# Optimization experiments

Hardware: AMD Instinct MI355X
Metric: run time of the kernel (lower is better)

The kernel has to match this reference:

```python
import jax, jax.numpy as jnp
import numpy as np

NB, NX, NU, NY, NQ = 16384, 512, 256, 128, 256


def setup_inputs() -> dict:
    key = jax.random.key(0)
    ks = jax.random.split(key, 13)
    s = 0.02  # small weight scale keeps the tanh recurrence well-behaved
    x = jax.random.normal(ks[0], (NB, NX), jnp.float32)
    u = jax.random.normal(ks[1], (NB, NU), jnp.float32)
    F = jax.random.normal(ks[2], (NX, NX), jnp.float32) * s
    B1 = jax.random.normal(ks[3], (NX, NQ), jnp.float32) * s
    B2 = jax.random.normal(ks[4], (NX, NU), jnp.float32) * s
    C1 = jax.random.normal(ks[5], (NQ, NX), jnp.float32) * s
    C2 = jax.random.normal(ks[6], (NY, NX), jnp.float32) * s
    D11 = jax.random.normal(ks[7], (NQ, NQ), jnp.float32) * s
    D12 = jax.random.normal(ks[8], (NQ, NU), jnp.float32) * s
    D21 = jax.random.normal(ks[9], (NY, NQ), jnp.float32) * s
    # E must be invertible (torch.inverse(self.E)); identity + small perturbation
    E = jnp.eye(NX, dtype=jnp.float32) + 0.05 * jax.random.normal(ks[10], (NX, NX), jnp.float32)
    # Lambda diagonal, positive (only Lambda[k,k] is used in _solve_w)
    lam = jax.random.uniform(ks[11], (NQ,), jnp.float32, minval=0.5, maxval=1.5)
    bv = jnp.zeros((NQ,), jnp.float32)  # bias=False -> bv is zeros
    return dict(x=x, u=u, F=F, B1=B1, B2=B2, C1=C1, C2=C2, D11=D11,
                D12=D12, D21=D21, E=E, lam=lam, bv=bv)


def _solve_w(x, u, C1, D11, D12, lam, bv):
    # Sequential forward-substitution over the nq nonlinear states:
    #   v_k = (x@C1[k] + w@D11[k] + u@D12[k] + bv[k]) / Lambda[k,k];  w_k = tanh(v_k)
    nb = x.shape[0]
    nq = lam.shape[0]
    # x/u contributions do not depend on w: precompute once. [nb, nq]
    xu = x @ C1.T + u @ D12.T + bv[None, :]

    def step(w, inp):
        d11_row, xu_k, lam_k, k = inp
        v_k = (xu_k + w @ d11_row) / lam_k          # [nb]
        w = w.at[:, k].set(jnp.tanh(v_k))
        return w, None

    w0 = jnp.zeros((nb, nq), x.dtype)
    w, _ = jax.lax.scan(step, w0, (D11, xu.T, lam, jnp.arange(nq)))
    return w


def reference(x, u, F, B1, B2, C1, C2, D11, D12, D21, E, lam, bv):
    w = _solve_w(x, u, C1, D11, D12, lam, bv)
    E_inv = jnp.linalg.inv(E)
    dx = x @ (E_inv @ F).T + w @ (E_inv @ B1).T + u @ (E_inv @ B2).T
    # linear_output path (no feedthrough: D22 term omitted as in default D22=0)
    y = x @ C2.T + w @ D21.T
    return dx, y
```

## Files before the change

kernel.cpp:

```cpp
#include <hip/hip_runtime.h>

#define NBq 16384
#define NXq 512
#define NUq 256
#define NYq 128
#define NQq 256
#define KP  1024
#define AUGW 1536

typedef __attribute__((ext_vector_type(8))) short short8;
typedef __attribute__((ext_vector_type(4))) float f32x4;

__device__ __forceinline__ ushort f2bf(float f) {
  uint x = __float_as_uint(f);
  x += 0x7FFFu + ((x >> 16) & 1u);
  return (ushort)(x >> 16);
}

#define GLOAD_LDS16(g, l)                                             \
  __builtin_amdgcn_global_load_lds(                                   \
      (const __attribute__((address_space(1))) void*)(g),             \
      (__attribute__((address_space(3))) void*)(l), 16, 0, 0)

__device__ __forceinline__ float rdlane(float x, int l) {
// ... 24 lines not shown
      int row = i >> 6, c4 = i & 63;
      ushort4 h = { f2bf(v.x), f2bf(v.y), f2bf(v.z), f2bf(v.w) };
      *(ushort4*)(P + (size_t)row * KP + 768 + c4 * 4) = h;
    }
  } else if (b < 15360) {
    int idx = (b - 12288) * 256 + tid;
    int r = idx / AUGW, c = idx % AUGW;
    float v;
    if (c < 512)       v = E[r * 512 + c];
    else if (c < 1024) v = F[r * 512 + (c - 512)];
    else if (c < 1280) v = B1[r * 256 + (c - 1024)];
    else               v = B2[r * 256 + (c - 1280)];
    AUG[idx] = v;
  } else if (b < 16384) {
    int idx = (b - 15360) * 256 + tid;
    int r = idx >> 10, k = idx & 1023;
    float v;
    if (k < 512)      v = C1[r * 512 + k];
    else if (k < 768) v = 0.f;
    else              v = D12[r * 256 + (k - 768)];
    Wxu[idx] = f2bf(v);
  } else if (b < 16640) {
    int idx = (b - 16384) * 256 + tid;
    D11B[idx] = f2bf(D11[idx]);
  } else {
    int idx = (b - 16640) * 256 + tid;
    int j = idx >> 10, k = idx & 1023;
    float v;
    if (k < 512)      v = C2[j * 512 + k];
    else if (k < 768) v = D21[j * 256 + (k - 512)];
    else              v = 0.f;
    Wfull[(size_t)(512 + j) * KP + k] = f2bf(v);
  }
}

__global__ __launch_bounds__(256) void k_gj(const float* __restrict__ Ain, float* __restrict__ Aout,
                                            ushort* __restrict__ Wfull, int s, int last) {
  __shared__ float M[64][132];
  __shared__ float sP[64][68];
  __shared__ float sMC[64][68];
  __shared__ float pinv[16][17];
  const int tid = threadIdx.x;
  const int wave = tid >> 6, lane = tid & 63;
  const int s64 = s * 64, r0 = blockIdx.x * 64, c0 = (s + 1 + blockIdx.y) * 64;
  const int r2 = tid >> 2, cq = (tid & 3) * 16;
  const int R4 = (tid >> 4) * 4;
  const int C4 = (tid & 15) * 4;
  const int C8 = (tid & 15) * 8;

  float av4[4][4];
  #pragma unroll
  for (int r = 0; r < 4; ++r) {
    float4 v = *(const float4*)(Ain + (size_t)(r0 + R4 + r) * AUGW + c0 + C4);
    av4[r][0] = v.x; av4[r][1] = v.y; av4[r][2] = v.z; av4[r][3] = v.w;
  }
  #pragma unroll
  for (int c4 = 0; c4 < 4; ++c4) {
    *(float4*)(&sP[r2][cq + c4 * 4]) =
        *(const float4*)(Ain + (size_t)(s64 + r2) * AUGW + c0 + cq + c4 * 4);
    *(float4*)(&sMC[r2][cq + c4 * 4]) =
        *(const float4*)(Ain + (size_t)(r0 + r2) * AUGW + s64 + cq + c4 * 4);
    *(float4*)(&M[r2][cq + c4 * 4]) =
        *(const float4*)(Ain + (size_t)(s64 + r2) * AUGW + s64 + cq + c4 * 4);
  }
  #pragma unroll
  for (int c = 0; c < 16; ++c)
    M[r2][64 + cq + c] = (r2 == cq + c) ? 1.f : 0.f;
  __syncthreads();

  for (int t = 0; t < 4; ++t) {
    const int kt = t * 16;
    if (wave == 0) {
      const int cc = lane & 31;
      float q[16];
      #pragma unroll
      for (int r = 0; r < 16; ++r)
        q[r] = (cc < 16) ? M[kt + r][kt + cc] : ((r == cc - 16) ? 1.f : 0.f);
      #pragma unroll
      for (int p = 0; p < 16; ++p) {
        float piv = rdlane(q[p], p);
        float rp = __builtin_amdgcn_rcpf(piv);
        rp = rp * (2.f - piv * rp);
        float a[16];
        #pragma unroll
        for (int r = 0; r < 16; ++r) a[r] = rdlane(q[r], p);
        q[p] *= rp;
        #pragma unroll
        for (int r = 0; r < 16; ++r)
          if (r != p) q[r] = fmaf(-a[r], q[p], q[r]);
      }
      if (lane >= 16 && lane < 32) {
        #pragma unroll
        for (int r = 0; r < 16; ++r) pinv[r][lane - 16] = q[r];
      }
    }
    __syncthreads();
    {
      const int ri = tid >> 4, j0 = (tid & 15) * 8;
      float rr[8] = {};
      float a0[8], a1[8], p0, p1;
      p0 = pinv[ri][0];
      #pragma unroll
      for (int c = 0; c < 8; c += 4)
        *(float4*)(&a0[c]) = *(const float4*)(&M[kt][j0 + c]);
      #pragma unroll
      for (int k = 0; k < 16; k += 2) {
        p1 = pinv[ri][k + 1];
        #pragma unroll
        for (int c = 0; c < 8; c += 4)
          *(float4*)(&a1[c]) = *(const float4*)(&M[kt + k + 1][j0 + c]);
        #pragma unroll
        for (int c = 0; c < 8; ++c) rr[c] = fmaf(p0, a0[c], rr[c]);
        if (k + 2 < 16) {
          p0 = pinv[ri][k + 2];
          #pragma unroll
          for (int c = 0; c < 8; c += 4)
            *(float4*)(&a0[c]) = *(const float4*)(&M[kt + k + 2][j0 + c]);
        }
        #pragma unroll
        for (int c = 0; c < 8; ++c) rr[c] = fmaf(p1, a1[c], rr[c]);
      }
      __syncthreads();
      #pragma unroll
      for (int c = 0; c < 8; c += 4)
        *(float4*)(&M[kt + ri][j0 + c]) = make_float4(rr[c], rr[c+1], rr[c+2], rr[c+3]);
    }
    __syncthreads();
    {
      const bool act = (wave != t);
      float mult[4][16], o2[4][8];
      if (act) {
        #pragma unroll
        for (int r = 0; r < 4; ++r) {
          #pragma unroll
          for (int j = 0; j < 4; ++j) {
            float4 m4 = *(const float4*)(&M[R4 + r][kt + 4 * j]);
            mult[r][4*j+0] = m4.x; mult[r][4*j+1] = m4.y;
            mult[r][4*j+2] = m4.z; mult[r][4*j+3] = m4.w;
          }
          float4 a = *(const float4*)(&M[R4 + r][C8]);
          float4 b = *(const float4*)(&M[R4 + r][C8 + 4]);
          o2[r][0] = a.x; o2[r][1] = a.y; o2[r][2] = a.z; o2[r][3] = a.w;
          o2[r][4] = b.x; o2[r][5] = b.y; o2[r][6] = b.z; o2[r][7] = b.w;
        }
      }
      __syncthreads();
      if (act) {
        float rv[2][8];
        {
          float4 a = *(const float4*)(&M[kt][C8]);
          float4 b = *(const float4*)(&M[kt][C8 + 4]);
          rv[0][0] = a.x; rv[0][1] = a.y; rv[0][2] = a.z; rv[0][3] = a.w;
          rv[0][4] = b.x; rv[0][5] = b.y; rv[0][6] = b.z; rv[0][7] = b.w;
        }
        #pragma unroll
        for (int k = 0; k < 16; ++k) {
          if (k + 1 < 16) {
            float4 a = *(const float4*)(&M[kt + k + 1][C8]);
            float4 b = *(const float4*)(&M[kt + k + 1][C8 + 4]);
            rv[(k+1)&1][0] = a.x; rv[(k+1)&1][1] = a.y;
            rv[(k+1)&1][2] = a.z; rv[(k+1)&1][3] = a.w;
            rv[(k+1)&1][4] = b.x; rv[(k+1)&1][5] = b.y;
            rv[(k+1)&1][6] = b.z; rv[(k+1)&1][7] = b.w;
          }
          #pragma unroll
          for (int r = 0; r < 4; ++r)
            #pragma unroll
            for (int c = 0; c < 8; ++c)
              o2[r][c] = fmaf(-mult[r][k], rv[k&1][c], o2[r][c]);
        }
        #pragma unroll
        for (int r = 0; r < 4; ++r) {
          *(float4*)(&M[R4 + r][C8]) =
              make_float4(o2[r][0], o2[r][1], o2[r][2], o2[r][3]);
          *(float4*)(&M[R4 + r][C8 + 4]) =
              make_float4(o2[r][4], o2[r][5], o2[r][6], o2[r][7]);
        }
      }
    }
    __syncthreads();
  }

  #define LOADCH_PB(dv, sv, ch)                                             \
    do {                                                                    \
      const int q0_ = (ch) * 4;                                             \
      _Pragma("unroll")                                                     \
      for (int r_ = 0; r_ < 4; ++r_) {                                      \
        float4 d_ = *(const float4*)(&M[R4 + r_][64 + q0_]);                \
        dv[r_][0] = d_.x; dv[r_][1] = d_.y; dv[r_][2] = d_.z; dv[r_][3] = d_.w; \
      }                                                                     \
      _Pragma("unroll")                                                     \
      for (int j_ = 0; j_ < 4; ++j_) {                                      \
        float4 s_ = *(const float4*)(&sP[q0_ + j_][C4]);                    \
        sv[j_][0] = s_.x; sv[j_][1] = s_.y; sv[j_][2] = s_.z; sv[j_][3] = s_.w; \
      }                                                                     \
    } while (0)
  #define LOADCH_MC(dv, sv, ch)                                             \
    do {                                                                    \
      const int q0_ = (ch) * 4;                                             \
      _Pragma("unroll")                                                     \
      for (int r_ = 0; r_ < 4; ++r_) {                                      \
        float4 d_ = *(const float4*)(&sMC[R4 + r_][q0_]);                   \
        dv[r_][0] = d_.x; dv[r_][1] = d_.y; dv[r_][2] = d_.z; dv[r_][3] = d_.w; \
      }                                                                     \
      _Pragma("unroll")                                                     \
      for (int j_ = 0; j_ < 4; ++j_) {                                      \
        float4 s_ = *(const float4*)(&sP[q0_ + j_][C4]);                    \
        sv[j_][0] = s_.x; sv[j_][1] = s_.y; sv[j_][2] = s_.z; sv[j_][3] = s_.w; \
      }                                                                     \
    } while (0)
  #define FMACH(acc, dv, sv, sgn)                                           \
    do {                                                                    \
      _Pragma("unroll")                                                     \
      for (int j_ = 0; j_ < 4; ++j_)                                        \
        _Pragma("unroll")                                                   \
        for (int r_ = 0; r_ < 4; ++r_)                                      \
          _Pragma("unroll")                                                 \
          for (int c_ = 0; c_ < 4; ++c_)                                    \
            acc[r_][c_] = fmaf(sgn dv[r_][j_], sv[j_][c_], acc[r_][c_]);    \
    } while (0)

  float pb[4][4] = {{0.f}};
  {
    float dvA[4][4], svA[4][4], dvB[4][4], svB[4][4];
    LOADCH_PB(dvA, svA, 0);
    #pragma unroll
    for (int ch = 0; ch < 16; ch += 2) {
      LOADCH_PB(dvB, svB, ch + 1);
      FMACH(pb, dvA, svA, +);
      if (ch + 2 < 16) LOADCH_PB(dvA, svA, ch + 2);
      FMACH(pb, dvB, svB, +);
    }
  }
  __syncthreads();
  #pragma unroll
  for (int r = 0; r < 4; ++r)
    *(float4*)(&sP[R4 + r][C4]) = make_float4(pb[r][0], pb[r][1], pb[r][2], pb[r][3]);
  __syncthreads();

  float o[4][4];
  if (blockIdx.x == (unsigned)s) {
    #pragma unroll
    for (int r = 0; r < 4; ++r)
      #pragma unroll
      for (int c = 0; c < 4; ++c) o[r][c] = pb[r][c];
  } else {
    #pragma unroll
    for (int r = 0; r < 4; ++r)
      #pragma unroll
      for (int c = 0; c < 4; ++c) o[r][c] = av4[r][c];
    float dvA[4][4], svA[4][4], dvB[4][4], svB[4][4];
    LOADCH_MC(dvA, svA, 0);
    #pragma unroll
    for (int ch = 0; ch < 16; ch += 2) {
      LOADCH_MC(dvB, svB, ch + 1);
      FMACH(o, dvA, svA, -);
      if (ch + 2 < 16) LOADCH_MC(dvA, svA, ch + 2);
      FMACH(o, dvB, svB, -);
    }
  }
  #undef LOADCH_PB
  #undef LOADCH_MC
  #undef FMACH
  if (last) {
    int k0 = c0 - 512 + C4;
    #pragma unroll
    for (int r = 0; r < 4; ++r) {
      ushort4 h = { f2bf(o[r][0]), f2bf(o[r][1]), f2bf(o[r][2]), f2bf(o[r][3]) };
      *(ushort4*)(Wfull + (size_t)(r0 + R4 + r) * KP + k0) = h;
    }
  } else {
    #pragma unroll
    for (int r = 0; r < 4; ++r)
      *(float4*)(Aout + (size_t)(r0 + R4 + r) * AUGW + c0 + C4) =
          make_float4(o[r][0], o[r][1], o[r][2], o[r][3]);
  }
}

template<bool SPLIT>
__global__ __launch_bounds__(256) void k_gemm(const ushort* __restrict__ P, const ushort* __restrict__ W,
                                              float* __restrict__ out) {
  __shared__ ushort sA[3][128 * 32];
  __shared__ ushort sB[3][128 * 32];
  int tid = threadIdx.x;
  int lane = tid & 63, wave = tid >> 6;
  int wm = wave & 1, wn = wave >> 1;
  int m0 = blockIdx.x * 128;
  int n0 = blockIdx.y * 128;
  int r16 = lane & 15, kq = lane >> 4;
  int lrow = lane >> 2, lseg = lane & 3;
  const ushort* gA0 = P + (size_t)(m0 + wave * 32 + lrow) * KP + lseg * 8;
  const ushort* gA1 = gA0 + 16 * KP;
  const ushort* gB0 = W + (size_t)(n0 + wave * 32 + lrow) * KP + lseg * 8;
  const ushort* gB1 = gB0 + 16 * KP;

  #define STAGE_KB(bi, kb_)                                        \
    do {                                                           \
      GLOAD_LDS16(gA0 + (kb_) * 32, &sA[bi][wave * 1024]);         \
      GLOAD_LDS16(gA1 + (kb_) * 32, &sA[bi][wave * 1024 + 512]);   \
      GLOAD_LDS16(gB0 + (kb_) * 32, &sB[bi][wave * 1024]);         \
      GLOAD_LDS16(gB1 + (kb_) * 32, &sB[bi][wave * 1024 + 512]);   \
    } while (0)

  f32x4 acc[4][4] = {};
  const int NKB = KP / 32;
  STAGE_KB(0, 0);
  STAGE_KB(1, 1);
  #pragma unroll
  for (int kb = 0; kb < NKB; ++kb) {
    const int bi = kb % 3;
    if (kb + 2 < NKB) {
      STAGE_KB((kb + 2) % 3, kb + 2);
      asm volatile("s_waitcnt vmcnt(8)" ::: "memory");
    } else if (kb + 2 == NKB) {
      asm volatile("s_waitcnt vmcnt(4)" ::: "memory");
    } else {
      asm volatile("s_waitcnt vmcnt(0)" ::: "memory");
    }
    __builtin_amdgcn_s_barrier();
    __builtin_amdgcn_sched_barrier(0);
    short8 af[4], bf[4];
    #pragma unroll
    for (int t = 0; t < 4; ++t) {
      af[t] = *(const short8*)(&sA[bi][(wm * 64 + t * 16 + r16) * 32 + kq * 8]);
      bf[t] = *(const short8*)(&sB[bi][(wn * 64 + t * 16 + r16) * 32 + kq * 8]);
    }
    #pragma unroll
    for (int mt = 0; mt < 4; ++mt)
      #pragma unroll
      for (int nt = 0; nt < 4; ++nt)
        acc[mt][nt] = __builtin_amdgcn_mfma_f32_16x16x32_bf16(af[mt], bf[nt], acc[mt][nt], 0, 0, 0);
    __builtin_amdgcn_sched_barrier(0);
    __builtin_amdgcn_s_barrier();
  }
  #undef STAGE_KB

  #pragma unroll
  for (int mt = 0; mt < 4; ++mt)
    #pragma unroll
    for (int nt = 0; nt < 4; ++nt)
      #pragma unroll
      for (int i = 0; i < 4; ++i) {
        int m = m0 + wm * 64 + mt * 16 + kq * 4 + i;
        int n = n0 + wn * 64 + nt * 16 + r16;
        float val = acc[mt][nt][i];
        if (SPLIT) {
          if (n < NXq) out[(size_t)m * NXq + n] = val;
          else out[(size_t)NBq * NXq + (size_t)m * NYq + (n - NXq)] = val;
        } else {
          out[(size_t)m * NQq + n] = val;
        }
      }
}

#define WSTRIDE 264
#define TANH_K 2.8853900817779268f

struct Pre {
  f32x4 xuv;
  short8 b[8];
  f32x4 rl2, bv2;
};

template<int t>
__device__ __forceinline__ void tile_loads(const float* __restrict__ xu,
                                           const ushort* __restrict__ D11B,
                                           const float* __restrict__ lam,
                                           const float* __restrict__ bv,
                                           int lane, int r0w, Pre& pre) {
  constexpr int kt = t * 16;
  constexpr int cmax = (t + 1) >> 1;
  const int mr = lane & 15, kq = lane >> 4, q = lane & 3;
  pre.xuv = *(const f32x4*)(&xu[(size_t)(r0w + mr) * NQq + kt + kq * 4]);
  #pragma unroll
  for (int c = 0; c < cmax; ++c)
    pre.b[c] = *(const short8*)(D11B + (size_t)(kt + mr) * NQq + c * 32 + kq * 8);
  float4 l4 = *(const float4*)(&lam[kt + q * 4]);
  float4 b4 = *(const float4*)(&bv[kt + q * 4]);
  pre.rl2[0] = TANH_K / l4.x; pre.rl2[1] = TANH_K / l4.y;
  pre.rl2[2] = TANH_K / l4.z; pre.rl2[3] = TANH_K / l4.w;
  pre.bv2[0] = b4.x * pre.rl2[0]; pre.bv2[1] = b4.y * pre.rl2[1];
  pre.bv2[2] = b4.z * pre.rl2[2]; pre.bv2[3] = b4.w * pre.rl2[3];
}

#define SOLVE_STEP(k, dvreg)                                                   \
// ... 42 lines not shown
  acc[3] = __int_as_float(__builtin_amdgcn_ds_bpermute(bp4, __float_as_int(accM[3])));
  const f32x4 rl2 = cur.rl2, bv2 = cur.bv2;
  float wreg = 0.f, wk[4] = {0.f, 0.f, 0.f, 0.f};
  {
    float v_ = fmaf(acc[0], rl2[0], bv2[0]);
    float e_ = __builtin_amdgcn_exp2f(v_);
    float w_ = fmaf(-2.f, __builtin_amdgcn_rcpf(1.f + e_), 1.f);
    wreg = w_;
    if (q == 0) wk[0] = w_;
  }
  SOLVE_STEP(1, dvb0)
  SOLVE_STEP(2, dvb1)
  SOLVE_STEP(3, dvb2)
  SOLVE_STEP(4, dvb3)
  SOLVE_STEP(5, dvb0)
  SOLVE_STEP(6, dvb1)
  SOLVE_STEP(7, dvb2)
  SOLVE_STEP(8, dvb3)
  SOLVE_STEP(9, dvb0)
  SOLVE_STEP(10, dvb1)
  SOLVE_STEP(11, dvb2)
  SOLVE_STEP(12, dvb3)
  SOLVE_STEP(13, dvb0)
  SOLVE_STEP(14, dvb1)
  SOLVE_STEP(15, dvb2)
  ushort4 h = { f2bf(wk[0]), f2bf(wk[1]), f2bf(wk[2]), f2bf(wk[3]) };
  *(ushort4*)(wb + r2 * WSTRIDE + kt + q * 4) = h;
  if (((lane >> 4) >> 1) == (t & 1)) {
    constexpr int c = t >> 1;
    whiF[c] = *(const short8*)(wb + (lane & 15) * WSTRIDE + c * 32 + (lane >> 4) * 8);
  }
}

__global__ __launch_bounds__(256) void k_solve(const float* __restrict__ xu,
                                               const float* __restrict__ D11,
                                               const ushort* __restrict__ D11B,
                                               const float* __restrict__ lam,
                                               const float* __restrict__ bv,
                                               ushort* __restrict__ P) {
  __shared__ ushort wB[4][16 * WSTRIDE];
  __shared__ float d11T[16][16][16];
  const int tid = threadIdx.x;
  const int wave = tid >> 6, lane = tid & 63;
  const int r0w = blockIdx.x * 64 + wave * 16;
  const int bp4 = (((lane >> 2) | ((lane & 3) << 4)) << 2);
  for (int i = tid; i < 4096; i += 256) {
    int tt = i >> 8, j = (i >> 4) & 15, c = i & 15;
    d11T[tt][j][c] = (c > j) ? D11[(size_t)(tt * 16 + c) * NQq + tt * 16 + j] : 0.f;
  }
  Pre pre0, pre1;
  tile_loads<0>(xu, D11B, lam, bv, lane, r0w, pre0);
  __syncthreads();
  ushort* wb = &wB[wave][0];
  short8 whiF[8] = {};
  do_tile<0>(xu, D11B, lam, bv, wb, d11T, whiF, lane, bp4, r0w, pre0, pre1);
  do_tile<1>(xu, D11B, lam, bv, wb, d11T, whiF, lane, bp4, r0w, pre1, pre0);
  do_tile<2>(xu, D11B, lam, bv, wb, d11T, whiF, lane, bp4, r0w, pre0, pre1);
  do_tile<3>(xu, D11B, lam, bv, wb, d11T, whiF, lane, bp4, r0w, pre1, pre0);
  do_tile<4>(xu, D11B, lam, bv, wb, d11T, whiF, lane, bp4, r0w, pre0, pre1);
  do_tile<5>(xu, D11B, lam, bv, wb, d11T, whiF, lane, bp4, r0w, pre1, pre0);
  do_tile<6>(xu, D11B, lam, bv, wb, d11T, whiF, lane, bp4, r0w, pre0, pre1);
  do_tile<7>(xu, D11B, lam, bv, wb, d11T, whiF, lane, bp4, r0w, pre1, pre0);
  do_tile<8>(xu, D11B, lam, bv, wb, d11T, whiF, lane, bp4, r0w, pre0, pre1);
  do_tile<9>(xu, D11B, lam, bv, wb, d11T, whiF, lane, bp4, r0w, pre1, pre0);
  do_tile<10>(xu, D11B, lam, bv, wb, d11T, whiF, lane, bp4, r0w, pre0, pre1);
  do_tile<11>(xu, D11B, lam, bv, wb, d11T, whiF, lane, bp4, r0w, pre1, pre0);
  do_tile<12>(xu, D11B, lam, bv, wb, d11T, whiF, lane, bp4, r0w, pre0, pre1);
  do_tile<13>(xu, D11B, lam, bv, wb, d11T, whiF, lane, bp4, r0w, pre1, pre0);
  do_tile<14>(xu, D11B, lam, bv, wb, d11T, whiF, lane, bp4, r0w, pre0, pre1);
  do_tile<15>(xu, D11B, lam, bv, wb, d11T, whiF, lane, bp4, r0w, pre1, pre0);
  #pragma unroll
  for (int it = 0; it < 8; ++it) {
    int f = it * 64 + lane;
    int m = f >> 5, k8 = f & 31;
    uint4 v = *(const uint4*)(wb + m * WSTRIDE + k8 * 8);
    *(uint4*)(P + (size_t)(r0w + m) * KP + NXq + k8 * 8) = v;
  }
}

extern "C" void kernel_launch(void* const* d_in, const int* in_sizes, int n_in,
                              void* d_out, int out_size, void* d_ws, size_t ws_size,
                              hipStream_t stream) {
  const float* x   = (const float*)d_in[0];
  const float* u   = (const float*)d_in[1];
  const float* F   = (const float*)d_in[2];
  const float* B1  = (const float*)d_in[3];
  const float* B2  = (const float*)d_in[4];
  const float* C1  = (const float*)d_in[5];
  const float* C2  = (const float*)d_in[6];
  const float* D11 = (const float*)d_in[7];
  const float* D12 = (const float*)d_in[8];
  const float* D21 = (const float*)d_in[9];
  const float* E   = (const float*)d_in[10];
  const float* lam = (const float*)d_in[11];
  const float* bv  = (const float*)d_in[12];

  char* ws = (char*)d_ws;
  ushort* P    = (ushort*)ws;
  float* xu    = (float*)(ws + (size_t)(32u << 20));
  float* AUG0  = (float*)(ws + (size_t)(48u << 20));
  float* AUG1  = (float*)(ws + (size_t)(52u << 20));
  ushort* Wfull = (ushort*)(ws + (size_t)(56u << 20));
  ushort* Wxu   = (ushort*)(ws + (size_t)(58u << 20));
  ushort* D11B  = (ushort*)(ws + (size_t)(59u << 20));
  float* out   = (float*)d_out;
  float* AUGbuf[2] = { AUG0, AUG1 };

  k_prep<<<17152, 256, 0, stream>>>(x, u, E, F, B1, B2, C1, C2, D11, D12, D21,
                                    P, AUG0, Wxu, D11B, Wfull);
  for (int s = 0; s < 8; ++s)
    k_gj<<<dim3(8, 23 - s), 256, 0, stream>>>(AUGbuf[s & 1], AUGbuf[(s + 1) & 1],
                                              Wfull, s, s == 7);
  k_gemm<false><<<dim3(128, 2), 256, 0, stream>>>(P, Wxu, xu);
  k_solve<<<256, 256, 0, stream>>>(xu, D11, D11B, lam, bv, P);
  k_gemm<true><<<dim3(128, 5), 256, 0, stream>>>(P, Wfull, out);
}
```

Before: 364.2 us.

## Overlap xu GEMM and w-solve with Gauss-Jordan inversion steps via fused kernel

Merges the Gauss-Jordan step kernel, the xu GEMM and the sequential w-solve into one launch per inversion step. Each launch uses a fixed 8x32 grid: blocks beyond the GJ tiles take extra work slices, chosen by a per-step offset table, so the independent xu GEMM and solve run alongside the E-inverse computation instead of after it. This fills idle CUs in the later, shrinking GJ steps and removes two launches. The cost is a larger shared-memory footprint for the fused kernel, which may lower occupancy, and a dependency on the solve slices running only after their xu tiles are written.

```diff
diff --git a/kernel.cpp b/kernel.cpp
--- a/kernel.cpp
+++ b/kernel.cpp
@@ -80,325 +80,6 @@
     else              v = 0.f;
     Wfull[(size_t)(512 + j) * KP + k] = f2bf(v);
   }
-}
-
-__global__ __launch_bounds__(256) void k_gj(const float* __restrict__ Ain, float* __restrict__ Aout,
-                                            ushort* __restrict__ Wfull, int s, int last) {
-  __shared__ float M[64][132];
-  __shared__ float sP[64][68];
-  __shared__ float sMC[64][68];
-  __shared__ float pinv[16][17];
-  const int tid = threadIdx.x;
-  const int wave = tid >> 6, lane = tid & 63;
-  const int s64 = s * 64, r0 = blockIdx.x * 64, c0 = (s + 1 + blockIdx.y) * 64;
-  const int r2 = tid >> 2, cq = (tid & 3) * 16;
-  const int R4 = (tid >> 4) * 4;
-  const int C4 = (tid & 15) * 4;
-  const int C8 = (tid & 15) * 8;
-
-  float av4[4][4];
-  #pragma unroll
-  for (int r = 0; r < 4; ++r) {
-    float4 v = *(const float4*)(Ain + (size_t)(r0 + R4 + r) * AUGW + c0 + C4);
-    av4[r][0] = v.x; av4[r][1] = v.y; av4[r][2] = v.z; av4[r][3] = v.w;
-  }
-  #pragma unroll
-  for (int c4 = 0; c4 < 4; ++c4) {
-    *(float4*)(&sP[r2][cq + c4 * 4]) =
-        *(const float4*)(Ain + (size_t)(s64 + r2) * AUGW + c0 + cq + c4 * 4);
-    *(float4*)(&sMC[r2][cq + c4 * 4]) =
-        *(const float4*)(Ain + (size_t)(r0 + r2) * AUGW + s64 + cq + c4 * 4);
-    *(float4*)(&M[r2][cq + c4 * 4]) =
-        *(const float4*)(Ain + (size_t)(s64 + r2) * AUGW + s64 + cq + c4 * 4);
-  }
-  #pragma unroll
-  for (int c = 0; c < 16; ++c)
-    M[r2][64 + cq + c] = (r2 == cq + c) ? 1.f : 0.f;
-  __syncthreads();
-
-  for (int t = 0; t < 4; ++t) {
-    const int kt = t * 16;
-    if (wave == 0) {
-      const int cc = lane & 31;
-      float q[16];
-      #pragma unroll
-      for (int r = 0; r < 16; ++r)
-        q[r] = (cc < 16) ? M[kt + r][kt + cc] : ((r == cc - 16) ? 1.f : 0.f);
-      #pragma unroll
-      for (int p = 0; p < 16; ++p) {
-        float piv = rdlane(q[p], p);
-        float rp = __builtin_amdgcn_rcpf(piv);
-        rp = rp * (2.f - piv * rp);
-        float a[16];
-        #pragma unroll
-        for (int r = 0; r < 16; ++r) a[r] = rdlane(q[r], p);
-        q[p] *= rp;
-        #pragma unroll
-        for (int r = 0; r < 16; ++r)
-          if (r != p) q[r] = fmaf(-a[r], q[p], q[r]);
-      }
-      if (lane >= 16 && lane < 32) {
-        #pragma unroll
-        for (int r = 0; r < 16; ++r) pinv[r][lane - 16] = q[r];
-      }
-    }
-    __syncthreads();
-    {
-      const int ri = tid >> 4, j0 = (tid & 15) * 8;
-      float rr[8] = {};
-      float a0[8], a1[8], p0, p1;
-      p0 = pinv[ri][0];
-      #pragma unroll
-      for (int c = 0; c < 8; c += 4)
-        *(float4*)(&a0[c]) = *(const float4*)(&M[kt][j0 + c]);
-      #pragma unroll
-      for (int k = 0; k < 16; k += 2) {
-        p1 = pinv[ri][k + 1];
-        #pragma unroll
-        for (int c = 0; c < 8; c += 4)
-          *(float4*)(&a1[c]) = *(const float4*)(&M[kt + k + 1][j0 + c]);
-        #pragma unroll
-        for (int c = 0; c < 8; ++c) rr[c] = fmaf(p0, a0[c], rr[c]);
-        if (k + 2 < 16) {
-          p0 = pinv[ri][k + 2];
-          #pragma unroll
-          for (int c = 0; c < 8; c += 4)
-            *(float4*)(&a0[c]) = *(const float4*)(&M[kt + k + 2][j0 + c]);
-        }
-        #pragma unroll
-        for (int c = 0; c < 8; ++c) rr[c] = fmaf(p1, a1[c], rr[c]);
-      }
-      __syncthreads();
-      #pragma unroll
-      for (int c = 0; c < 8; c += 4)
-        *(float4*)(&M[kt + ri][j0 + c]) = make_float4(rr[c], rr[c+1], rr[c+2], rr[c+3]);
-    }
-    __syncthreads();
-    {
-      const bool act = (wave != t);
-      float mult[4][16], o2[4][8];
-      if (act) {
-        #pragma unroll
-        for (int r = 0; r < 4; ++r) {
-          #pragma unroll
-          for (int j = 0; j < 4; ++j) {
-            float4 m4 = *(const float4*)(&M[R4 + r][kt + 4 * j]);
-            mult[r][4*j+0] = m4.x; mult[r][4*j+1] = m4.y;
-            mult[r][4*j+2] = m4.z; mult[r][4*j+3] = m4.w;
-          }
-          float4 a = *(const float4*)(&M[R4 + r][C8]);
-          float4 b = *(const float4*)(&M[R4 + r][C8 + 4]);
-          o2[r][0] = a.x; o2[r][1] = a.y; o2[r][2] = a.z; o2[r][3] = a.w;
-          o2[r][4] = b.x; o2[r][5] = b.y; o2[r][6] = b.z; o2[r][7] = b.w;
-        }
-      }
-      __syncthreads();
-      if (act) {
-        float rv[2][8];
-        {
-          float4 a = *(const float4*)(&M[kt][C8]);
-          float4 b = *(const float4*)(&M[kt][C8 + 4]);
-          rv[0][0] = a.x; rv[0][1] = a.y; rv[0][2] = a.z; rv[0][3] = a.w;
-          rv[0][4] = b.x; rv[0][5] = b.y; rv[0][6] = b.z; rv[0][7] = b.w;
-        }
-        #pragma unroll
-        for (int k = 0; k < 16; ++k) {
-          if (k + 1 < 16) {
-            float4 a = *(const float4*)(&M[kt + k + 1][C8]);
-            float4 b = *(const float4*)(&M[kt + k + 1][C8 + 4]);
-            rv[(k+1)&1][0] = a.x; rv[(k+1)&1][1] = a.y;
-            rv[(k+1)&1][2] = a.z; rv[(k+1)&1][3] = a.w;
-            rv[(k+1)&1][4] = b.x; rv[(k+1)&1][5] = b.y;
-            rv[(k+1)&1][6] = b.z; rv[(k+1)&1][7] = b.w;
-          }
-          #pragma unroll
-          for (int r = 0; r < 4; ++r)
-            #pragma unroll
-            for (int c = 0; c < 8; ++c)
-              o2[r][c] = fmaf(-mult[r][k], rv[k&1][c], o2[r][c]);
-        }
-        #pragma unroll
-        for (int r = 0; r < 4; ++r) {
-          *(float4*)(&M[R4 + r][C8]) =
-              make_float4(o2[r][0], o2[r][1], o2[r][2], o2[r][3]);
-          *(float4*)(&M[R4 + r][C8 + 4]) =
-              make_float4(o2[r][4], o2[r][5], o2[r][6], o2[r][7]);
-        }
-      }
-    }
-    __syncthreads();
-  }
-
-  #define LOADCH_PB(dv, sv, ch)                                             \
-    do {                                                                    \
-      const int q0_ = (ch) * 4;                                             \
-      _Pragma("unroll")                                                     \
-      for (int r_ = 0; r_ < 4; ++r_) {                                      \
-        float4 d_ = *(const float4*)(&M[R4 + r_][64 + q0_]);                \
-        dv[r_][0] = d_.x; dv[r_][1] = d_.y; dv[r_][2] = d_.z; dv[r_][3] = d_.w; \
-      }                                                                     \
-      _Pragma("unroll")                                                     \
-      for (int j_ = 0; j_ < 4; ++j_) {                                      \
-        float4 s_ = *(const float4*)(&sP[q0_ + j_][C4]);                    \
-        sv[j_][0] = s_.x; sv[j_][1] = s_.y; sv[j_][2] = s_.z; sv[j_][3] = s_.w; \
-      }                                                                     \
-    } while (0)
-  #define LOADCH_MC(dv, sv, ch)                                             \
-    do {                                                                    \
-      const int q0_ = (ch) * 4;                                             \
-      _Pragma("unroll")                                                     \
-      for (int r_ = 0; r_ < 4; ++r_) {                                      \
-        float4 d_ = *(const float4*)(&sMC[R4 + r_][q0_]);                   \
-        dv[r_][0] = d_.x; dv[r_][1] = d_.y; dv[r_][2] = d_.z; dv[r_][3] = d_.w; \
-      }                                                                     \
-      _Pragma("unroll")                                                     \
-      for (int j_ = 0; j_ < 4; ++j_) {                                      \
-        float4 s_ = *(const float4*)(&sP[q0_ + j_][C4]);                    \
-        sv[j_][0] = s_.x; sv[j_][1] = s_.y; sv[j_][2] = s_.z; sv[j_][3] = s_.w; \
-      }                                                                     \
-    } while (0)
-  #define FMACH(acc, dv, sv, sgn)                                           \
-    do {                                                                    \
-      _Pragma("unroll")                                                     \
-      for (int j_ = 0; j_ < 4; ++j_)                                        \
-        _Pragma("unroll")                                                   \
-        for (int r_ = 0; r_ < 4; ++r_)                                      \
-          _Pragma("unroll")                                                 \
-          for (int c_ = 0; c_ < 4; ++c_)                                    \
-            acc[r_][c_] = fmaf(sgn dv[r_][j_], sv[j_][c_], acc[r_][c_]);    \
-    } while (0)
-
-  float pb[4][4] = {{0.f}};
-  {
-    float dvA[4][4], svA[4][4], dvB[4][4], svB[4][4];
-    LOADCH_PB(dvA, svA, 0);
-    #pragma unroll
-    for (int ch = 0; ch < 16; ch += 2) {
-      LOADCH_PB(dvB, svB, ch + 1);
-      FMACH(pb, dvA, svA, +);
-      if (ch + 2 < 16) LOADCH_PB(dvA, svA, ch + 2);
-      FMACH(pb, dvB, svB, +);
-    }
-  }
-  __syncthreads();
-  #pragma unroll
-  for (int r = 0; r < 4; ++r)
-    *(float4*)(&sP[R4 + r][C4]) = make_float4(pb[r][0], pb[r][1], pb[r][2], pb[r][3]);
-  __syncthreads();
-
-  float o[4][4];
-  if (blockIdx.x == (unsigned)s) {
-    #pragma unroll
-    for (int r = 0; r < 4; ++r)
-      #pragma unroll
-      for (int c = 0; c < 4; ++c) o[r][c] = pb[r][c];
-  } else {
-    #pragma unroll
-    for (int r = 0; r < 4; ++r)
-      #pragma unroll
-      for (int c = 0; c < 4; ++c) o[r][c] = av4[r][c];
-    float dvA[4][4], svA[4][4], dvB[4][4], svB[4][4];
-    LOADCH_MC(dvA, svA, 0);
-    #pragma unroll
-    for (int ch = 0; ch < 16; ch += 2) {
-      LOADCH_MC(dvB, svB, ch + 1);
-      FMACH(o, dvA, svA, -);
-      if (ch + 2 < 16) LOADCH_MC(dvA, svA, ch + 2);
-      FMACH(o, dvB, svB, -);
-    }
-  }
-  #undef LOADCH_PB
-  #undef LOADCH_MC
-  #undef FMACH
-  if (last) {
-    int k0 = c0 - 512 + C4;
-    #pragma unroll
-    for (int r = 0; r < 4; ++r) {
-      ushort4 h = { f2bf(o[r][0]), f2bf(o[r][1]), f2bf(o[r][2]), f2bf(o[r][3]) };
-      *(ushort4*)(Wfull + (size_t)(r0 + R4 + r) * KP + k0) = h;
-    }
-  } else {
-    #pragma unroll
-    for (int r = 0; r < 4; ++r)
-      *(float4*)(Aout + (size_t)(r0 + R4 + r) * AUGW + c0 + C4) =
-          make_float4(o[r][0], o[r][1], o[r][2], o[r][3]);
-  }
-}
-
-template<bool SPLIT>
-__global__ __launch_bounds__(256) void k_gemm(const ushort* __restrict__ P, const ushort* __restrict__ W,
-                                              float* __restrict__ out) {
-  __shared__ ushort sA[3][128 * 32];
-  __shared__ ushort sB[3][128 * 32];
-  int tid = threadIdx.x;
-  int lane = tid & 63, wave = tid >> 6;
-  int wm = wave & 1, wn = wave >> 1;
-  int m0 = blockIdx.x * 128;
-  int n0 = blockIdx.y * 128;
-  int r16 = lane & 15, kq = lane >> 4;
-  int lrow = lane >> 2, lseg = lane & 3;
-  const ushort* gA0 = P + (size_t)(m0 + wave * 32 + lrow) * KP + lseg * 8;
-  const ushort* gA1 = gA0 + 16 * KP;
-  const ushort* gB0 = W + (size_t)(n0 + wave * 32 + lrow) * KP + lseg * 8;
-  const ushort* gB1 = gB0 + 16 * KP;
-
-  #define STAGE_KB(bi, kb_)                                        \
-    do {                                                           \
-      GLOAD_LDS16(gA0 + (kb_) * 32, &sA[bi][wave * 1024]);         \
-      GLOAD_LDS16(gA1 + (kb_) * 32, &sA[bi][wave * 1024 + 512]);   \
-      GLOAD_LDS16(gB0 + (kb_) * 32, &sB[bi][wave * 1024]);         \
-      GLOAD_LDS16(gB1 + (kb_) * 32, &sB[bi][wave * 1024 + 512]);   \
-    } while (0)
-
-  f32x4 acc[4][4] = {};
-  const int NKB = KP / 32;
-  STAGE_KB(0, 0);
-  STAGE_KB(1, 1);
-  #pragma unroll
-  for (int kb = 0; kb < NKB; ++kb) {
-    const int bi = kb % 3;
-    if (kb + 2 < NKB) {
-      STAGE_KB((kb + 2) % 3, kb + 2);
-      asm volatile("s_waitcnt vmcnt(8)" ::: "memory");
-    } else if (kb + 2 == NKB) {
-      asm volatile("s_waitcnt vmcnt(4)" ::: "memory");
-    } else {
-      asm volatile("s_waitcnt vmcnt(0)" ::: "memory");
-    }
-    __builtin_amdgcn_s_barrier();
-    __builtin_amdgcn_sched_barrier(0);
-    short8 af[4], bf[4];
-    #pragma unroll
-    for (int t = 0; t < 4; ++t) {
-      af[t] = *(const short8*)(&sA[bi][(wm * 64 + t * 16 + r16) * 32 + kq * 8]);
-      bf[t] = *(const short8*)(&sB[bi][(wn * 64 + t * 16 + r16) * 32 + kq * 8]);
-    }
-    #pragma unroll
-    for (int mt = 0; mt < 4; ++mt)
-      #pragma unroll
-      for (int nt = 0; nt < 4; ++nt)
-        acc[mt][nt] = __builtin_amdgcn_mfma_f32_16x16x32_bf16(af[mt], bf[nt], acc[mt][nt], 0, 0, 0);
-    __builtin_amdgcn_sched_barrier(0);
-    __builtin_amdgcn_s_barrier();
-  }
-  #undef STAGE_KB
-
-  #pragma unroll
-  for (int mt = 0; mt < 4; ++mt)
-    #pragma unroll
-    for (int nt = 0; nt < 4; ++nt)
-      #pragma unroll
-      for (int i = 0; i < 4; ++i) {
-        int m = m0 + wm * 64 + mt * 16 + kq * 4 + i;
-        int n = n0 + wn * 64 + nt * 16 + r16;
-        float val = acc[mt][nt][i];
-        if (SPLIT) {
-          if (n < NXq) out[(size_t)m * NXq + n] = val;
-          else out[(size_t)NBq * NXq + (size_t)m * NYq + (n - NXq)] = val;
-        } else {
-          out[(size_t)m * NQq + n] = val;
-        }
-      }
 }
 
 #define WSTRIDE 264
@@ -507,50 +188,441 @@
   }
 }
 
-__global__ __launch_bounds__(256) void k_solve(const float* __restrict__ xu,
+__global__ __launch_bounds__(256) void k_fused(const float* __restrict__ Ain, float* __restrict__ Aout,
+                                               ushort* __restrict__ Wfull, int s, int ebase,
+                                               ushort* __restrict__ P, const ushort* __restrict__ Wxu,
+                                               float* __restrict__ xu,
                                                const float* __restrict__ D11,
                                                const ushort* __restrict__ D11B,
                                                const float* __restrict__ lam,
-                                               const float* __restrict__ bv,
-                                               ushort* __restrict__ P) {
-  __shared__ ushort wB[4][16 * WSTRIDE];
-  __shared__ float d11T[16][16][16];
+                                               const float* __restrict__ bv) {
+  __shared__ __align__(16) char smem[69696];
   const int tid = threadIdx.x;
   const int wave = tid >> 6, lane = tid & 63;
-  const int r0w = blockIdx.x * 64 + wave * 16;
-  const int bp4 = (((lane >> 2) | ((lane & 3) << 4)) << 2);
-  for (int i = tid; i < 4096; i += 256) {
-    int tt = i >> 8, j = (i >> 4) & 15, c = i & 15;
-    d11T[tt][j][c] = (c > j) ? D11[(size_t)(tt * 16 + c) * NQq + tt * 16 + j] : 0.f;
-  }
-  Pre pre0, pre1;
-  tile_loads<0>(xu, D11B, lam, bv, lane, r0w, pre0);
-  __syncthreads();
-  ushort* wb = &wB[wave][0];
-  short8 whiF[8] = {};
-  do_tile<0>(xu, D11B, lam, bv, wb, d11T, whiF, lane, bp4, r0w, pre0, pre1);
-  do_tile<1>(xu, D11B, lam, bv, wb, d11T, whiF, lane, bp4, r0w, pre1, pre0);
-  do_tile<2>(xu, D11B, lam, bv, wb, d11T, whiF, lane, bp4, r0w, pre0, pre1);
-  do_tile<3>(xu, D11B, lam, bv, wb, d11T, whiF, lane, bp4, r0w, pre1, pre0);
-  do_tile<4>(xu, D11B, lam, bv, wb, d11T, whiF, lane, bp4, r0w, pre0, pre1);
-  do_tile<5>(xu, D11B, lam, bv, wb, d11T, whiF, lane, bp4, r0w, pre1, pre0);
-  do_tile<6>(xu, D11B, lam, bv, wb, d11T, whiF, lane, bp4, r0w, pre0, pre1);
-  do_tile<7>(xu, D11B, lam, bv, wb, d11T, whiF, lane, bp4, r0w, pre1, pre0);
-  do_tile<8>(xu, D11B, lam, bv, wb, d11T, whiF, lane, bp4, r0w, pre0, pre1);
-  do_tile<9>(xu, D11B, lam, bv, wb, d11T, whiF, lane, bp4, r0w, pre1, pre0);
-  do_tile<10>(xu, D11B, lam, bv, wb, d11T, whiF, lane, bp4, r0w, pre0, pre1);
-  do_tile<11>(xu, D11B, lam, bv, wb, d11T, whiF, lane, bp4, r0w, pre1, pre0);
-  do_tile<12>(xu, D11B, lam, bv, wb, d11T, whiF, lane, bp4, r0w, pre0, pre1);
-  do_tile<13>(xu, D11B, lam, bv, wb, d11T, whiF, lane, bp4, r0w, pre1, pre0);
-  do_tile<14>(xu, D11B, lam, bv, wb, d11T, whiF, lane, bp4, r0w, pre0, pre1);
-  do_tile<15>(xu, D11B, lam, bv, wb, d11T, whiF, lane, bp4, r0w, pre1, pre0);
+  const int nby = 23 - s;
+  const int last = (s == 7);
+
+  if ((int)blockIdx.y < nby) {
+    float (*M)[132] = (float (*)[132])smem;
+    float (*sP)[68] = (float (*)[68])(smem + 33792);
+    float (*sMC)[68] = (float (*)[68])(smem + 33792 + 17408);
+    float (*pinv)[17] = (float (*)[17])(smem + 33792 + 2 * 17408);
+    const int s64 = s * 64, r0 = blockIdx.x * 64, c0 = (s + 1 + blockIdx.y) * 64;
+    const int r2 = tid >> 2, cq = (tid & 3) * 16;
+    const int R4 = (tid >> 4) * 4;
+    const int C4 = (tid & 15) * 4;
+    const int C8 = (tid & 15) * 8;
+
+    float av4[4][4];
+    #pragma unroll
+    for (int r = 0; r < 4; ++r) {
+      float4 v = *(const float4*)(Ain + (size_t)(r0 + R4 + r) * AUGW + c0 + C4);
+      av4[r][0] = v.x; av4[r][1] = v.y; av4[r][2] = v.z; av4[r][3] = v.w;
+    }
+    #pragma unroll
+    for (int c4 = 0; c4 < 4; ++c4) {
+      *(float4*)(&sP[r2][cq + c4 * 4]) =
+          *(const float4*)(Ain + (size_t)(s64 + r2) * AUGW + c0 + cq + c4 * 4);
+      *(float4*)(&sMC[r2][cq + c4 * 4]) =
+          *(const float4*)(Ain + (size_t)(r0 + r2) * AUGW + s64 + cq + c4 * 4);
+      *(float4*)(&M[r2][cq + c4 * 4]) =
+          *(const float4*)(Ain + (size_t)(s64 + r2) * AUGW + s64 + cq + c4 * 4);
+    }
+    #pragma unroll
+    for (int c = 0; c < 16; ++c)
+      M[r2][64 + cq + c] = (r2 == cq + c) ? 1.f : 0.f;
+    __syncthreads();
+
+    for (int t = 0; t < 4; ++t) {
+      const int kt = t * 16;
+      if (wave == 0) {
+        const int cc = lane & 31;
+        float q[16];
+        #pragma unroll
+        for (int r = 0; r < 16; ++r)
+          q[r] = (cc < 16) ? M[kt + r][kt + cc] : ((r == cc - 16) ? 1.f : 0.f);
+        #pragma unroll
+        for (int p = 0; p < 16; ++p) {
+          float piv = rdlane(q[p], p);
+          float rp = __builtin_amdgcn_rcpf(piv);
+          rp = rp * (2.f - piv * rp);
+          float a[16];
+          #pragma unroll
+          for (int r = 0; r < 16; ++r) a[r] = rdlane(q[r], p);
+          q[p] *= rp;
+          #pragma unroll
+          for (int r = 0; r < 16; ++r)
+            if (r != p) q[r] = fmaf(-a[r], q[p], q[r]);
+        }
+        if (lane >= 16 && lane < 32) {
+          #pragma unroll
+          for (int r = 0; r < 16; ++r) pinv[r][lane - 16] = q[r];
+        }
+      }
+      __syncthreads();
+      {
+        const int ri = tid >> 4, j0 = (tid & 15) * 8;
+        float rr[8] = {};
+        float a0[8], a1[8], p0, p1;
+        p0 = pinv[ri][0];
+        #pragma unroll
+        for (int c = 0; c < 8; c += 4)
+          *(float4*)(&a0[c]) = *(const float4*)(&M[kt][j0 + c]);
+        #pragma unroll
+        for (int k = 0; k < 16; k += 2) {
+          p1 = pinv[ri][k + 1];
+          #pragma unroll
+          for (int c = 0; c < 8; c += 4)
+            *(float4*)(&a1[c]) = *(const float4*)(&M[kt + k + 1][j0 + c]);
+          #pragma unroll
+          for (int c = 0; c < 8; ++c) rr[c] = fmaf(p0, a0[c], rr[c]);
+          if (k + 2 < 16) {
+            p0 = pinv[ri][k + 2];
+            #pragma unroll
+            for (int c = 0; c < 8; c += 4)
+              *(float4*)(&a0[c]) = *(const float4*)(&M[kt + k + 2][j0 + c]);
+          }
+          #pragma unroll
+          for (int c = 0; c < 8; ++c) rr[c] = fmaf(p1, a1[c], rr[c]);
+        }
+        __syncthreads();
+        #pragma unroll
+        for (int c = 0; c < 8; c += 4)
+          *(float4*)(&M[kt + ri][j0 + c]) = make_float4(rr[c], rr[c+1], rr[c+2], rr[c+3]);
+      }
+      __syncthreads();
+      {
+        const bool act = (wave != t);
+        float mult[4][16], o2[4][8];
+        if (act) {
+          #pragma unroll
+          for (int r = 0; r < 4; ++r) {
+            #pragma unroll
+            for (int j = 0; j < 4; ++j) {
+              float4 m4 = *(const float4*)(&M[R4 + r][kt + 4 * j]);
+              mult[r][4*j+0] = m4.x; mult[r][4*j+1] = m4.y;
+              mult[r][4*j+2] = m4.z; mult[r][4*j+3] = m4.w;
+            }
+            float4 a = *(const float4*)(&M[R4 + r][C8]);
+            float4 b = *(const float4*)(&M[R4 + r][C8 + 4]);
+            o2[r][0] = a.x; o2[r][1] = a.y; o2[r][2] = a.z; o2[r][3] = a.w;
+            o2[r][4] = b.x; o2[r][5] = b.y; o2[r][6] = b.z; o2[r][7] = b.w;
+          }
+        }
+        __syncthreads();
+        if (act) {
+          float rv[2][8];
+          {
+            float4 a = *(const float4*)(&M[kt][C8]);
+            float4 b = *(const float4*)(&M[kt][C8 + 4]);
+            rv[0][0] = a.x; rv[0][1] = a.y; rv[0][2] = a.z; rv[0][3] = a.w;
+            rv[0][4] = b.x; rv[0][5] = b.y; rv[0][6] = b.z; rv[0][7] = b.w;
+          }
+          #pragma unroll
+          for (int k = 0; k < 16; ++k) {
+            if (k + 1 < 16) {
+              float4 a = *(const float4*)(&M[kt + k + 1][C8]);
+              float4 b = *(const float4*)(&M[kt + k + 1][C8 + 4]);
+              rv[(k+1)&1][0] = a.x; rv[(k+1)&1][1] = a.y;
+              rv[(k+1)&1][2] = a.z; rv[(k+1)&1][3] = a.w;
+              rv[(k+1)&1][4] = b.x; rv[(k+1)&1][5] = b.y;
+              rv[(k+1)&1][6] = b.z; rv[(k+1)&1][7] = b.w;
+            }
+            #pragma unroll
+            for (int r = 0; r < 4; ++r)
+              #pragma unroll
+              for (int c = 0; c < 8; ++c)
+                o2[r][c] = fmaf(-mult[r][k], rv[k&1][c], o2[r][c]);
+          }
+          #pragma unroll
+          for (int r = 0; r < 4; ++r) {
+            *(float4*)(&M[R4 + r][C8]) =
+                make_float4(o2[r][0], o2[r][1], o2[r][2], o2[r][3]);
+            *(float4*)(&M[R4 + r][C8 + 4]) =
+                make_float4(o2[r][4], o2[r][5], o2[r][6], o2[r][7]);
+          }
+        }
+      }
+      __syncthreads();
+    }
+
+    #define LOADCH_PB(dv, sv, ch)                                             \
+      do {                                                                    \
+        const int q0_ = (ch) * 4;                                             \
+        _Pragma("unroll")                                                     \
+        for (int r_ = 0; r_ < 4; ++r_) {                                      \
+          float4 d_ = *(const float4*)(&M[R4 + r_][64 + q0_]);                \
+          dv[r_][0] = d_.x; dv[r_][1] = d_.y; dv[r_][2] = d_.z; dv[r_][3] = d_.w; \
+        }                                                                     \
+        _Pragma("unroll")                                                     \
+        for (int j_ = 0; j_ < 4; ++j_) {                                      \
+          float4 s_ = *(const float4*)(&sP[q0_ + j_][C4]);                    \
+          sv[j_][0] = s_.x; sv[j_][1] = s_.y; sv[j_][2] = s_.z; sv[j_][3] = s_.w; \
+        }                                                                     \
+      } while (0)
+    #define LOADCH_MC(dv, sv, ch)                                             \
+      do {                                                                    \
+        const int q0_ = (ch) * 4;                                             \
+        _Pragma("unroll")                                                     \
+        for (int r_ = 0; r_ < 4; ++r_) {                                      \
+          float4 d_ = *(const float4*)(&sMC[R4 + r_][q0_]);                   \
+          dv[r_][0] = d_.x; dv[r_][1] = d_.y; dv[r_][2] = d_.z; dv[r_][3] = d_.w; \
+        }                                                                     \
+        _Pragma("unroll")                                                     \
+        for (int j_ = 0; j_ < 4; ++j_) {                                      \
+          float4 s_ = *(const float4*)(&sP[q0_ + j_][C4]);                    \
+          sv[j_][0] = s_.x; sv[j_][1] = s_.y; sv[j_][2] = s_.z; sv[j_][3] = s_.w; \
+        }                                                                     \
+      } while (0)
+    #define FMACH(acc, dv, sv, sgn)                                           \
+      do {                                                                    \
+        _Pragma("unroll")                                                     \
+        for (int j_ = 0; j_ < 4; ++j_)                                        \
+          _Pragma("unroll")                                                   \
+          for (int r_ = 0; r_ < 4; ++r_)                                      \
+            _Pragma("unroll")                                                 \
+            for (int c_ = 0; c_ < 4; ++c_)                                    \
+              acc[r_][c_] = fmaf(sgn dv[r_][j_], sv[j_][c_], acc[r_][c_]);    \
+      } while (0)
+
+    float pb[4][4] = {{0.f}};
+    {
+      float dvA[4][4], svA[4][4], dvB[4][4], svB[4][4];
+      LOADCH_PB(dvA, svA, 0);
+      #pragma unroll
+      for (int ch = 0; ch < 16; ch += 2) {
+        LOADCH_PB(dvB, svB, ch + 1);
+        FMACH(pb, dvA, svA, +);
+        if (ch + 2 < 16) LOADCH_PB(dvA, svA, ch + 2);
+        FMACH(pb, dvB, svB, +);
+      }
+    }
+    __syncthreads();
+    #pragma unroll
+    for (int r = 0; r < 4; ++r)
+      *(float4*)(&sP[R4 + r][C4]) = make_float4(pb[r][0], pb[r][1], pb[r][2], pb[r][3]);
+    __syncthreads();
+
+    float o[4][4];
+    if (blockIdx.x == (unsigned)s) {
+      #pragma unroll
+      for (int r = 0; r < 4; ++r)
+        #pragma unroll
+        for (int c = 0; c < 4; ++c) o[r][c] = pb[r][c];
+    } else {
+      #pragma unroll
+      for (int r = 0; r < 4; ++r)
+        #pragma unroll
+        for (int c = 0; c < 4; ++c) o[r][c] = av4[r][c];
+      float dvA[4][4], svA[4][4], dvB[4][4], svB[4][4];
+      LOADCH_MC(dvA, svA, 0);
+      #pragma unroll
+      for (int ch = 0; ch < 16; ch += 2) {
+        LOADCH_MC(dvB, svB, ch + 1);
+        FMACH(o, dvA, svA, -);
+        if (ch + 2 < 16) LOADCH_MC(dvA, svA, ch + 2);
+        FMACH(o, dvB, svB, -);
+      }
+    }
+    #undef LOADCH_PB
+    #undef LOADCH_MC
+    #undef FMACH
+    if (last) {
+      int k0 = c0 - 512 + C4;
+      #pragma unroll
+      for (int r = 0; r < 4; ++r) {
+        ushort4 h = { f2bf(o[r][0]), f2bf(o[r][1]), f2bf(o[r][2]), f2bf(o[r][3]) };
+        *(ushort4*)(Wfull + (size_t)(r0 + R4 + r) * KP + k0) = h;
+      }
+    } else {
+      #pragma unroll
+      for (int r = 0; r < 4; ++r)
+        *(float4*)(Aout + (size_t)(r0 + R4 + r) * AUGW + c0 + C4) =
+            make_float4(o[r][0], o[r][1], o[r][2], o[r][3]);
+    }
+    return;
+  }
+
+  const int g = ebase + ((int)blockIdx.y - nby) * 8 + (int)blockIdx.x;
+
+  if (g < 256) {
+    ushort* sA = (ushort*)smem;
+    ushort* sB = (ushort*)(smem + 24576);
+    const int mb = g >> 1, nb = g & 1;
+    int wm = wave & 1, wn = wave >> 1;
+    int m0 = mb * 128, n0 = nb * 128;
+    int r16 = lane & 15, kq = lane >> 4;
+    int lrow = lane >> 2, lseg = lane & 3;
+    const ushort* gA0 = P + (size_t)(m0 + wave * 32 + lrow) * KP + lseg * 8;
+    const ushort* gA1 = gA0 + 16 * KP;
+    const ushort* gB0 = Wxu + (size_t)(n0 + wave * 32 + lrow) * KP + lseg * 8;
+    const ushort* gB1 = gB0 + 16 * KP;
+
+    #define STAGE_KB(bi, kb_)                                              \
+      do {                                                                 \
+        GLOAD_LDS16(gA0 + (kb_) * 32, sA + (bi) * 4096 + wave * 1024);     \
+        GLOAD_LDS16(gA1 + (kb_) * 32, sA + (bi) * 4096 + wave * 1024 + 512); \
+        GLOAD_LDS16(gB0 + (kb_) * 32, sB + (bi) * 4096 + wave * 1024);     \
+        GLOAD_LDS16(gB1 + (kb_) * 32, sB + (bi) * 4096 + wave * 1024 + 512); \
+      } while (0)
+
+    f32x4 acc[4][4] = {};
+    const int NKB = KP / 32;
+    STAGE_KB(0, 0);
+    STAGE_KB(1, 1);
+    #pragma unroll
+    for (int kb = 0; kb < NKB; ++kb) {
+      const int bi = kb % 3;
+      if (kb + 2 < NKB) {
+        STAGE_KB((kb + 2) % 3, kb + 2);
+        asm volatile("s_waitcnt vmcnt(8)" ::: "memory");
+      } else if (kb + 2 == NKB) {
+        asm volatile("s_waitcnt vmcnt(4)" ::: "memory");
+      } else {
+        asm volatile("s_waitcnt vmcnt(0)" ::: "memory");
+      }
+      __builtin_amdgcn_s_barrier();
+      __builtin_amdgcn_sched_barrier(0);
+      short8 af[4], bf[4];
+      #pragma unroll
+      for (int t = 0; t < 4; ++t) {
+        af[t] = *(const short8*)(sA + bi * 4096 + (wm * 64 + t * 16 + r16) * 32 + kq * 8);
+        bf[t] = *(const short8*)(sB + bi * 4096 + (wn * 64 + t * 16 + r16) * 32 + kq * 8);
+      }
+      #pragma unroll
+      for (int mt = 0; mt < 4; ++mt)
+        #pragma unroll
+        for (int nt = 0; nt < 4; ++nt)
+          acc[mt][nt] = __builtin_amdgcn_mfma_f32_16x16x32_bf16(af[mt], bf[nt], acc[mt][nt], 0, 0, 0);
+      __builtin_amdgcn_sched_barrier(0);
+      __builtin_amdgcn_s_barrier();
+    }
+    #undef STAGE_KB
+
+    #pragma unroll
+    for (int mt = 0; mt < 4; ++mt)
+      #pragma unroll
+      for (int nt = 0; nt < 4; ++nt)
+        #pragma unroll
+        for (int i = 0; i < 4; ++i) {
+          int m = m0 + wm * 64 + mt * 16 + kq * 4 + i;
+          int n = n0 + wn * 64 + nt * 16 + r16;
+          xu[(size_t)m * NQq + n] = acc[mt][nt][i];
+        }
+    return;
+  }
+
+  if (g >= 336 && g < 592) {
+    const int sid = g - 336;
+    ushort* wB = (ushort*)smem;
+    float (*d11T)[16][16] = (float (*)[16][16])(smem + 33792);
+    const int r0w = sid * 64 + wave * 16;
+    const int bp4 = (((lane >> 2) | ((lane & 3) << 4)) << 2);
+    for (int i = tid; i < 4096; i += 256) {
+      int tt = i >> 8, j = (i >> 4) & 15, c = i & 15;
+      d11T[tt][j][c] = (c > j) ? D11[(size_t)(tt * 16 + c) * NQq + tt * 16 + j] : 0.f;
+    }
+    Pre pre0, pre1;
+    tile_loads<0>(xu, D11B, lam, bv, lane, r0w, pre0);
+    __syncthreads();
+    ushort* wb = wB + wave * 16 * WSTRIDE;
+    short8 whiF[8] = {};
+    do_tile<0>(xu, D11B, lam, bv, wb, d11T, whiF, lane, bp4, r0w, pre0, pre1);
+    do_tile<1>(xu, D11B, lam, bv, wb, d11T, whiF, lane, bp4, r0w, pre1, pre0);
+    do_tile<2>(xu, D11B, lam, bv, wb, d11T, whiF, lane, bp4, r0w, pre0, pre1);
+    do_tile<3>(xu, D11B, lam, bv, wb, d11T, whiF, lane, bp4, r0w, pre1, pre0);
+    do_tile<4>(xu, D11B, lam, bv, wb, d11T, whiF, lane, bp4, r0w, pre0, pre1);
+    do_tile<5>(xu, D11B, lam, bv, wb, d11T, whiF, lane, bp4, r0w, pre1, pre0);
+    do_tile<6>(xu, D11B, lam, bv, wb, d11T, whiF, lane, bp4, r0w, pre0, pre1);
+    do_tile<7>(xu, D11B, lam, bv, wb, d11T, whiF, lane, bp4, r0w, pre1, pre0);
+    do_tile<8>(xu, D11B, lam, bv, wb, d11T, whiF, lane, bp4, r0w, pre0, pre1);
+    do_tile<9>(xu, D11B, lam, bv, wb, d11T, whiF, lane, bp4, r0w, pre1, pre0);
+    do_tile<10>(xu, D11B, lam, bv, wb, d11T, whiF, lane, bp4, r0w, pre0, pre1);
+    do_tile<11>(xu, D11B, lam, bv, wb, d11T, whiF, lane, bp4, r0w, pre1, pre0);
+    do_tile<12>(xu, D11B, lam, bv, wb, d11T, whiF, lane, bp4, r0w, pre0, pre1);
+    do_tile<13>(xu, D11B, lam, bv, wb, d11T, whiF, lane, bp4, r0w, pre1, pre0);
+    do_tile<14>(xu, D11B, lam, bv, wb, d11T, whiF, lane, bp4, r0w, pre0, pre1);
+    do_tile<15>(xu, D11B, lam, bv, wb, d11T, whiF, lane, bp4, r0w, pre1, pre0);
+    #pragma unroll
+    for (int it = 0; it < 8; ++it) {
+      int f = it * 64 + lane;
+      int m = f >> 5, k8 = f & 31;
+      uint4 v = *(const uint4*)(wb + m * WSTRIDE + k8 * 8);
+      *(uint4*)(P + (size_t)(r0w + m) * KP + NXq + k8 * 8) = v;
+    }
+    return;
+  }
+}
+
+__global__ __launch_bounds__(256) void k_gemm(const ushort* __restrict__ P, const ushort* __restrict__ W,
+                                              float* __restrict__ out) {
+  __shared__ ushort sA[3][128 * 32];
+  __shared__ ushort sB[3][128 * 32];
+  int tid = threadIdx.x;
+  int lane = tid & 63, wave = tid >> 6;
+  int wm = wave & 1, wn = wave >> 1;
+  int m0 = blockIdx.x * 128;
+  int n0 = blockIdx.y * 128;
+  int r16 = lane & 15, kq = lane >> 4;
+  int lrow = lane >> 2, lseg = lane & 3;
+  const ushort* gA0 = P + (size_t)(m0 + wave * 32 + lrow) * KP + lseg * 8;
+  const ushort* gA1 = gA0 + 16 * KP;
+  const ushort* gB0 = W + (size_t)(n0 + wave * 32 + lrow) * KP + lseg * 8;
+  const ushort* gB1 = gB0 + 16 * KP;
+
+  #define STAGE_KB(bi, kb_)                                        \
+    do {                                                           \
+      GLOAD_LDS16(gA0 + (kb_) * 32, &sA[bi][wave * 1024]);         \
+      GLOAD_LDS16(gA1 + (kb_) * 32, &sA[bi][wave * 1024 + 512]);   \
+      GLOAD_LDS16(gB0 + (kb_) * 32, &sB[bi][wave * 1024]);         \
+      GLOAD_LDS16(gB1 + (kb_) * 32, &sB[bi][wave * 1024 + 512]);   \
+    } while (0)
+
+  f32x4 acc[4][4] = {};
+  const int NKB = KP / 32;
+  STAGE_KB(0, 0);
+  STAGE_KB(1, 1);
   #pragma unroll
-  for (int it = 0; it < 8; ++it) {
-    int f = it * 64 + lane;
-    int m = f >> 5, k8 = f & 31;
-    uint4 v = *(const uint4*)(wb + m * WSTRIDE + k8 * 8);
-    *(uint4*)(P + (size_t)(r0w + m) * KP + NXq + k8 * 8) = v;
-  }
+  for (int kb = 0; kb < NKB; ++kb) {
+    const int bi = kb % 3;
+    if (kb + 2 < NKB) {
+      STAGE_KB((kb + 2) % 3, kb + 2);
+      asm volatile("s_waitcnt vmcnt(8)" ::: "memory");
+    } else if (kb + 2 == NKB) {
+      asm volatile("s_waitcnt vmcnt(4)" ::: "memory");
+    } else {
+      asm volatile("s_waitcnt vmcnt(0)" ::: "memory");
+    }
+    __builtin_amdgcn_s_barrier();
+    __builtin_amdgcn_sched_barrier(0);
+    short8 af[4], bf[4];
+    #pragma unroll
+    for (int t = 0; t < 4; ++t) {
+      af[t] = *(const short8*)(&sA[bi][(wm * 64 + t * 16 + r16) * 32 + kq * 8]);
+      bf[t] = *(const short8*)(&sB[bi][(wn * 64 + t * 16 + r16) * 32 + kq * 8]);
+    }
+    #pragma unroll
+    for (int mt = 0; mt < 4; ++mt)
+      #pragma unroll
+      for (int nt = 0; nt < 4; ++nt)
+        acc[mt][nt] = __builtin_amdgcn_mfma_f32_16x16x32_bf16(af[mt], bf[nt], acc[mt][nt], 0, 0, 0);
+    __builtin_amdgcn_sched_barrier(0);
+    __builtin_amdgcn_s_barrier();
+  }
+  #undef STAGE_KB
+
+  #pragma unroll
+  for (int mt = 0; mt < 4; ++mt)
+    #pragma unroll
+    for (int nt = 0; nt < 4; ++nt)
+      #pragma unroll
+      for (int i = 0; i < 4; ++i) {
+        int m = m0 + wm * 64 + mt * 16 + kq * 4 + i;
+        int n = n0 + wn * 64 + nt * 16 + r16;
+        float val = acc[mt][nt][i];
+        if (n < NXq) out[(size_t)m * NXq + n] = val;
+        else out[(size_t)NBq * NXq + (size_t)m * NYq + (n - NXq)] = val;
+      }
 }
 
 extern "C" void kernel_launch(void* const* d_in, const int* in_sizes, int n_in,
@@ -581,12 +653,13 @@
   float* out   = (float*)d_out;
   float* AUGbuf[2] = { AUG0, AUG1 };
 
+  static const int ebase_tab[8] = {0, 72, 152, 240, 336, 440, 552, 672};
+
   k_prep<<<17152, 256, 0, stream>>>(x, u, E, F, B1, B2, C1, C2, D11, D12, D21,
                                     P, AUG0, Wxu, D11B, Wfull);
   for (int s = 0; s < 8; ++s)
-    k_gj<<<dim3(8, 23 - s), 256, 0, stream>>>(AUGbuf[s & 1], AUGbuf[(s + 1) & 1],
-                                              Wfull, s, s == 7);
-  k_gemm<false><<<dim3(128, 2), 256, 0, stream>>>(P, Wxu, xu);
-  k_solve<<<256, 256, 0, stream>>>(xu, D11, D11B, lam, bv, P);
-  k_gemm<true><<<dim3(128, 5), 256, 0, stream>>>(P, Wfull, out);
-}
+    k_fused<<<dim3(8, 32), 256, 0, stream>>>(AUGbuf[s & 1], AUGbuf[(s + 1) & 1],
+                                             Wfull, s, ebase_tab[s],
+                                             P, Wxu, xu, D11, D11B, lam, bv);
+  k_gemm<<<dim3(128, 5), 256, 0, stream>>>(P, Wfull, out);
+}
```

Result: faster. 325.4 us (median of 2 runs) (-10.7%).
